# Performance work log

Measured on AMD Instinct MI355X. Metric: run time of the kernel, lower is better.

The kernel has to match this reference:

```python
import jax, jax.numpy as jnp
import numpy as np

VOCAB = 100000
EMBED = 64
HIDDEN = 256
SEQ = 200
BATCH = 4096


def setup_inputs() -> dict:
    key = jax.random.key(0)
    ks = jax.random.split(key, 12)
    s = 0.02
    return {
        "user_hist": jax.random.randint(ks[0], (BATCH, SEQ), 0, VOCAB),
        "target_item": jax.random.randint(ks[1], (BATCH,), 0, VOCAB),
        "user_emb": jax.random.normal(ks[2], (VOCAB, EMBED), jnp.float32) * s,
        "item_emb": jax.random.normal(ks[3], (VOCAB, EMBED), jnp.float32) * s,
        "attn_w1": jax.random.normal(ks[4], (4 * EMBED, HIDDEN), jnp.float32) * s,
        "attn_b1": jnp.zeros((HIDDEN,), jnp.float32),
        "attn_w2": jax.random.normal(ks[5], (HIDDEN, 1), jnp.float32) * s,
        "attn_b2": jnp.zeros((1,), jnp.float32),
        "mlp_w1": jax.random.normal(ks[6], (2 * EMBED, HIDDEN), jnp.float32) * s,
        "mlp_b1": jnp.zeros((HIDDEN,), jnp.float32),
        "mlp_w2": jax.random.normal(ks[7], (HIDDEN, 1), jnp.float32) * s,
        "mlp_b2": jnp.zeros((1,), jnp.float32),
    }


def reference(user_hist, target_item, user_emb, item_emb,
              attn_w1, attn_b1, attn_w2, attn_b2,
              mlp_w1, mlp_b1, mlp_w2, mlp_b2):
    # [B, S, E] history embeddings, [B, 1, E] target embedding
    h = user_emb[user_hist]
    t = item_emb[target_item][:, None, :]
    tb = jnp.broadcast_to(t, h.shape)
    # attention MLP over [B, S, 4E]
    att_in = jnp.concatenate([h, tb, h - t, h * t], axis=-1)
    att_h = jax.nn.relu(att_in @ attn_w1 + attn_b1)
    att_logits = (att_h @ attn_w2 + attn_b2)[..., 0]            # [B, S]
    att_w = jax.nn.softmax(att_logits, axis=-1)[..., None]      # [B, S, 1]
    user_interest = jnp.sum(h * att_w, axis=1)                  # [B, E]
    # prediction head on [B, 2E]
    mlp_in = jnp.concatenate([user_interest, t[:, 0, :]], axis=-1)
    mlp_h = jax.nn.relu(mlp_in @ mlp_w1 + mlp_b1)
    out = jax.nn.sigmoid(mlp_h @ mlp_w2 + mlp_b2)               # [B, 1]
    return out
```

## Files before the change

kernel.cpp:

```cpp
#include <hip/hip_runtime.h>
#include <math.h>

#define EMBED   64
#define HIDDEN  256
#define SEQ     200
#define SEQP    208
#define MT      13

typedef _Float16 f16x8  __attribute__((ext_vector_type(8)));
typedef float    f32x4  __attribute__((ext_vector_type(4)));
typedef float    f32x2  __attribute__((ext_vector_type(2)));

__global__ void din_precompute(const float* __restrict__ attn_w1,
                               const float* __restrict__ mlp_w1,
                               uint2* __restrict__ fragB8,
                               _Float16* __restrict__ fragW3,
                               _Float16* __restrict__ fragDt,
                               _Float16* __restrict__ fragB2) {
  const int gid = blockIdx.x * 256 + threadIdx.x;
  if (gid < 2048) {
    const int i = gid >> 7, rem = gid & 127, kc = rem >> 6, lane = rem & 63;
    const int n = i * 16 + (lane & 15);
    const int kb = kc * 32 + (lane >> 4) * 8;
    float v[8];
    #pragma unroll
    for (int j = 0; j < 8; ++j)
      v[j] = 16.0f * (attn_w1[(kb + j) * HIDDEN + n] + attn_w1[(128 + kb + j) * HIDDEN + n]);
    int lo = __builtin_amdgcn_cvt_pk_fp8_f32(v[0], v[1], 0, false);
    lo     = __builtin_amdgcn_cvt_pk_fp8_f32(v[2], v[3], lo, true);
    int hi = __builtin_amdgcn_cvt_pk_fp8_f32(v[4], v[5], 0, false);
    hi     = __builtin_amdgcn_cvt_pk_fp8_f32(v[6], v[7], hi, true);
    fragB8[gid] = uint2{(unsigned)lo, (unsigned)hi};
  } else if (gid < 4096) {
    const int g = gid - 2048;
    const int i = g >> 7, rem = g & 127, kc = rem >> 6, lane = rem & 63;
    const int n = i * 16 + (lane & 15);
    const int kb = kc * 32 + (lane >> 4) * 8;
    #pragma unroll
    for (int j = 0; j < 8; ++j)
      fragW3[g * 8 + j] = (_Float16)(16.0f * attn_w1[(192 + kb + j) * HIDDEN + n]);
  } else if (gid < 6144) {
    const int g = gid - 4096;
    const int i = g >> 7, rem = g & 127, kc = rem >> 6, lane = rem & 63;
    const int n = i * 16 + (lane & 15);
    const int kb = kc * 32 + (lane >> 4) * 8;
    #pragma unroll
    for (int j = 0; j < 8; ++j)
      fragDt[g * 8 + j] = (_Float16)(attn_w1[(64 + kb + j) * HIDDEN + n]
                                   - attn_w1[(128 + kb + j) * HIDDEN + n]);
  } else {
    const int g = gid - 6144;
    const int nt = g >> 8, kc = (g >> 6) & 3, lane = g & 63;
    const int n = nt * 16 + (lane & 15);
    const int kb = kc * 32 + (lane >> 4) * 8;
    #pragma unroll
    for (int j = 0; j < 8; ++j)
      fragB2[g * 8 + j] = (_Float16)mlp_w1[(kb + j) * HIDDEN + n];
  }
}

__global__ __launch_bounds__(512, 8)
void din_fused_kernel(const int* __restrict__ user_hist,
                      const int* __restrict__ target_item,
                      const float* __restrict__ user_emb,
                      const float* __restrict__ item_emb,
                      const float* __restrict__ attn_b1,
                      const float* __restrict__ attn_w2,
                      const float* __restrict__ mlp_b1,
                      const float* __restrict__ mlp_w2,
                      const float* __restrict__ mlp_b2,
                      const uint2* __restrict__ fragB8,
                      const _Float16* __restrict__ fragW3,
                      const _Float16* __restrict__ fragDt,
                      const _Float16* __restrict__ fragB2,
                      float* __restrict__ out)
{
  __shared__ __align__(16) uint2 Hf8[MT * 2 * 64];
  __shared__ __align__(16) _Float16 t16[EMBED];
  __shared__ int   histL[SEQP];
  __shared__ float lp[8][SEQP];
  __shared__ float weights[SEQP];
  __shared__ __align__(16) _Float16 mi16[EMBED];
  __shared__ float red[16];

  const int b    = blockIdx.x;
  const int tid  = threadIdx.x;
  const int lane = tid & 63;
  const int wave = tid >> 6;
  const int m    = lane & 15;
  const int quad = lane >> 4;

  if (tid < EMBED) t16[tid] = (_Float16)item_emb[target_item[b] * EMBED + tid];
  if (tid < SEQP) histL[tid] = (tid < SEQ) ? user_hist[b * SEQ + tid] : 0;

  long long Aw8[2][2];
  #pragma unroll
  for (int i = 0; i < 2; ++i)
    #pragma unroll
    for (int c = 0; c < 2; ++c)
      Aw8[i][c] = __builtin_bit_cast(long long, fragB8[((2 * wave + i) * 2 + c) * 64 + lane]);
  __syncthreads();

  for (int slot = tid; slot < MT * 2 * 64; slot += 512) {
    const int ln = slot & 63, kcomb = slot >> 6;
    const int st = kcomb >> 1, kc = kcomb & 1;
    const int s = st * 16 + (ln & 15);
    const int kb = kc * 32 + (ln >> 4) * 8;
    uint2 pv = uint2{0u, 0u};
    if (s < SEQ) {
      const float4* src = reinterpret_cast<const float4*>(&user_emb[histL[s] * EMBED + kb]);
      const float4 x = src[0], y = src[1];
      int lo = __builtin_amdgcn_cvt_pk_fp8_f32(16.f * x.x, 16.f * x.y, 0, false);
      lo     = __builtin_amdgcn_cvt_pk_fp8_f32(16.f * x.z, 16.f * x.w, lo, true);
      int hi = __builtin_amdgcn_cvt_pk_fp8_f32(16.f * y.x, 16.f * y.y, 0, false);
      hi     = __builtin_amdgcn_cvt_pk_fp8_f32(16.f * y.z, 16.f * y.w, hi, true);
      pv = uint2{(unsigned)lo, (unsigned)hi};
    }
    Hf8[slot] = pv;
  }
  __syncthreads();

  const f16x8 tv0 = *reinterpret_cast<const f16x8*>(&t16[quad * 8]);
  const f16x8 tv1 = *reinterpret_cast<const f16x8*>(&t16[32 + quad * 8]);

  long long AwT[2][2];
  #pragma unroll
  for (int i = 0; i < 2; ++i) {
    #pragma unroll
    for (int c = 0; c < 2; ++c) {
      const f16x8 w3v = reinterpret_cast<const f16x8*>(fragW3)[((2 * wave + i) * 2 + c) * 64 + lane];
      const f16x8 p = w3v * (c ? tv1 : tv0);
      int lo = __builtin_amdgcn_cvt_pk_fp8_f32((float)p[0], (float)p[1], 0, false);
      lo     = __builtin_amdgcn_cvt_pk_fp8_f32((float)p[2], (float)p[3], lo, true);
      int hi = __builtin_amdgcn_cvt_pk_fp8_f32((float)p[4], (float)p[5], 0, false);
      hi     = __builtin_amdgcn_cvt_pk_fp8_f32((float)p[6], (float)p[7], hi, true);
      AwT[i][c] = __builtin_bit_cast(long long, uint2{(unsigned)lo, (unsigned)hi});
    }
  }

  float cn[2][4], w2n[2][4];
  #pragma unroll
  for (int i = 0; i < 2; ++i) {
    const int tile = 2 * wave + i;
    const f16x8 d0 = reinterpret_cast<const f16x8*>(fragDt)[(tile * 2 + 0) * 64 + lane];
    const f16x8 d1 = reinterpret_cast<const f16x8*>(fragDt)[(tile * 2 + 1) * 64 + lane];
    f32x4 acc = {0.f, 0.f, 0.f, 0.f};
    acc = __builtin_amdgcn_mfma_f32_16x16x32_f16(d0, tv0, acc, 0, 0, 0);
    acc = __builtin_amdgcn_mfma_f32_16x16x32_f16(d1, tv1, acc, 0, 0, 0);
    const int nb = tile * 16 + quad * 4;
    const float4 b1v = *reinterpret_cast<const float4*>(&attn_b1[nb]);
    const float4 w2v = *reinterpret_cast<const float4*>(&attn_w2[nb]);
    cn[i][0] = 256.0f * (b1v.x + acc[0]);
    cn[i][1] = 256.0f * (b1v.y + acc[1]);
    cn[i][2] = 256.0f * (b1v.z + acc[2]);
    cn[i][3] = 256.0f * (b1v.w + acc[3]);
    w2n[i][0] = w2v.x * (1.0f / 256.0f);
    w2n[i][1] = w2v.y * (1.0f / 256.0f);
    w2n[i][2] = w2v.z * (1.0f / 256.0f);
    w2n[i][3] = w2v.w * (1.0f / 256.0f);
  }

  #pragma unroll 4
  for (int st = 0; st < MT; ++st) {
    const long long b0 = __builtin_bit_cast(long long, Hf8[(st * 2 + 0) * 64 + lane]);
    const long long b1 = __builtin_bit_cast(long long, Hf8[(st * 2 + 1) * 64 + lane]);
    float lg = 0.f;
    #pragma unroll
    for (int i = 0; i < 2; ++i) {
      f32x4 acc = {cn[i][0], cn[i][1], cn[i][2], cn[i][3]};
      acc = __builtin_amdgcn_mfma_f32_16x16x32_fp8_fp8(Aw8[i][0], b0, acc, 0, 0, 0);
      acc = __builtin_amdgcn_mfma_f32_16x16x32_fp8_fp8(Aw8[i][1], b1, acc, 0, 0, 0);
      acc = __builtin_amdgcn_mfma_f32_16x16x32_fp8_fp8(AwT[i][0], b0, acc, 0, 0, 0);
      acc = __builtin_amdgcn_mfma_f32_16x16x32_fp8_fp8(AwT[i][1], b1, acc, 0, 0, 0);
      #pragma unroll
      for (int r = 0; r < 4; ++r)
        lg += fmaxf(acc[r], 0.0f) * w2n[i][r];
    }
    lg += __shfl_xor(lg, 16, 64);
    lg += __shfl_xor(lg, 32, 64);
    if (lane < 16) lp[wave][st * 16 + lane] = lg;
  }
  __syncthreads();

  float v = -INFINITY, e = 0.0f;
  if (wave < 4) {
    if (tid < SEQ)
      v = lp[0][tid] + lp[1][tid] + lp[2][tid] + lp[3][tid]
        + lp[4][tid] + lp[5][tid] + lp[6][tid] + lp[7][tid];
    float mx = v;
    #pragma unroll
    for (int off = 32; off; off >>= 1) mx = fmaxf(mx, __shfl_xor(mx, off, 64));
    if (lane == 0) red[wave] = mx;
  }
  __syncthreads();
  if (wave < 4) {
    const float mx = fmaxf(fmaxf(red[0], red[1]), fmaxf(red[2], red[3]));
    e = (tid < SEQ) ? expf(v - mx) : 0.0f;
    float ssum = e;
    #pragma unroll
    for (int off = 32; off; off >>= 1) ssum += __shfl_xor(ssum, off, 64);
    if (lane == 0) red[4 + wave] = ssum;
  }
  __syncthreads();
  if (wave < 4) {
    const float tot = red[4] + red[5] + red[6] + red[7];
    if (tid < SEQP) weights[tid] = (tid < SEQ) ? e / tot : 0.0f;
  }
  __syncthreads();

  {
    const int kc = wave & 1, g = wave >> 1;
    float pk[8];
    #pragma unroll
    for (int j = 0; j < 8; ++j) pk[j] = 0.f;
    #pragma unroll
    for (int st2 = 0; st2 < 4; ++st2) {
      const int st = g + st2 * 4;
      if (st < MT) {
        const float wt = weights[st * 16 + m];
        const uint2 hv = Hf8[(st * 2 + kc) * 64 + lane];
        const f32x2 f0 = __builtin_amdgcn_cvt_pk_f32_fp8((int)hv.x, false);
        const f32x2 f1 = __builtin_amdgcn_cvt_pk_f32_fp8((int)hv.x, true);
        const f32x2 f2 = __builtin_amdgcn_cvt_pk_f32_fp8((int)hv.y, false);
        const f32x2 f3 = __builtin_amdgcn_cvt_pk_f32_fp8((int)hv.y, true);
        pk[0] += wt * f0.x;  pk[1] += wt * f0.y;
        pk[2] += wt * f1.x;  pk[3] += wt * f1.y;
        pk[4] += wt * f2.x;  pk[5] += wt * f2.y;
        pk[6] += wt * f3.x;  pk[7] += wt * f3.y;
      }
    }
    #pragma unroll
    for (int j = 0; j < 8; ++j) {
      float p = pk[j];
      p += __shfl_xor(p, 1, 64);
      p += __shfl_xor(p, 2, 64);
      p += __shfl_xor(p, 4, 64);
      p += __shfl_xor(p, 8, 64);
      pk[j] = p;
    }
    if (m == 0) {
      #pragma unroll
      for (int j = 0; j < 8; ++j)
        lp[g][kc * 32 + quad * 8 + j] = pk[j];
    }
  }
  __syncthreads();
  if (tid < EMBED)
    mi16[tid] = (_Float16)((lp[0][tid] + lp[1][tid] + lp[2][tid] + lp[3][tid]) * 0.0625f);
  __syncthreads();

  {
    const f16x8 mb0 = *reinterpret_cast<const f16x8*>(&mi16[quad * 8]);
    const f16x8 mb1 = *reinterpret_cast<const f16x8*>(&mi16[32 + quad * 8]);
    float z = 0.f;
    #pragma unroll
    for (int i = 0; i < 2; ++i) {
      const f16x8* B2 = reinterpret_cast<const f16x8*>(fragB2) + ((2 * wave + i) * 4) * 64 + lane;
      const int nb = (2 * wave + i) * 16 + quad * 4;
      const float4 bb = *reinterpret_cast<const float4*>(&mlp_b1[nb]);
      const float4 ww = *reinterpret_cast<const float4*>(&mlp_w2[nb]);
      f32x4 acc = {bb.x, bb.y, bb.z, bb.w};
      acc = __builtin_amdgcn_mfma_f32_16x16x32_f16(B2[0],   mb0, acc, 0, 0, 0);
      acc = __builtin_amdgcn_mfma_f32_16x16x32_f16(B2[64],  mb1, acc, 0, 0, 0);
      acc = __builtin_amdgcn_mfma_f32_16x16x32_f16(B2[128], tv0, acc, 0, 0, 0);
      acc = __builtin_amdgcn_mfma_f32_16x16x32_f16(B2[192], tv1, acc, 0, 0, 0);
      z += fmaxf(acc[0], 0.0f) * ww.x;
      z += fmaxf(acc[1], 0.0f) * ww.y;
      z += fmaxf(acc[2], 0.0f) * ww.z;
      z += fmaxf(acc[3], 0.0f) * ww.w;
    }
    z += __shfl_xor(z, 16, 64);
    z += __shfl_xor(z, 32, 64);
    if (lane == 0) red[wave] = z;
  }
  __syncthreads();
  if (tid == 0) {
    const float zz = red[0] + red[1] + red[2] + red[3]
                   + red[4] + red[5] + red[6] + red[7] + mlp_b2[0];
    out[b] = 1.0f / (1.0f + expf(-zz));
  }
}

extern "C" void kernel_launch(void* const* d_in, const int* in_sizes, int n_in,
                              void* d_out, int out_size, void* d_ws, size_t ws_size,
                              hipStream_t stream) {
  const int*   user_hist   = (const int*)  d_in[0];
  const int*   target_item = (const int*)  d_in[1];
  const float* user_emb    = (const float*)d_in[2];
  const float* item_emb    = (const float*)d_in[3];
  const float* attn_w1     = (const float*)d_in[4];
  const float* attn_b1     = (const float*)d_in[5];
  const float* attn_w2     = (const float*)d_in[6];
  const float* mlp_w1      = (const float*)d_in[8];
  const float* mlp_b1      = (const float*)d_in[9];
  const float* mlp_w2      = (const float*)d_in[10];
  const float* mlp_b2      = (const float*)d_in[11];
  float* out = (float*)d_out;

  uint2*    fragB8 = (uint2*)d_ws;
  _Float16* fragW3 = (_Float16*)((char*)d_ws + 16384);
  _Float16* fragDt = (_Float16*)((char*)d_ws + 49152);
  _Float16* fragB2 = (_Float16*)((char*)d_ws + 81920);

  din_precompute<<<40, 256, 0, stream>>>(attn_w1, mlp_w1, fragB8, fragW3, fragDt, fragB2);

  const int batch = in_sizes[1];
  din_fused_kernel<<<batch, 512, 0, stream>>>(
      user_hist, target_item, user_emb, item_emb,
      attn_b1, attn_w2, mlp_b1, mlp_w2, mlp_b2,
      fragB8, fragW3, fragDt, fragB2, out);
}
```

Before: 180.3 us.

## Use K=128 scaled FP8 MFMA with h*t operand folded into history tile

Replaces the four 16x16x32 fp8 MFMAs per tile with one 16x16x128 scaled f8f6f4 MFMA, moving the h*t product into the activation side so that each history row stores both h and h*t in fp8 in padded LDS rows. The prediction head also becomes a single K=128 fp8 MFMA with pre-packed weights, and the per-wave logit partials are reduced through LDS atomics instead of a lp buffer. Weight preprocessing is consolidated into fewer fragment arrays. This doubles the LDS history footprint and quantizes the head input to fp8, which risks accuracy and occupancy.

```diff
diff --git a/kernel.cpp b/kernel.cpp
--- a/kernel.cpp
+++ b/kernel.cpp
@@ -6,56 +6,56 @@
 #define SEQ     200
 #define SEQP    208
 #define MT      13
-
-typedef _Float16 f16x8  __attribute__((ext_vector_type(8)));
-typedef float    f32x4  __attribute__((ext_vector_type(4)));
-typedef float    f32x2  __attribute__((ext_vector_type(2)));
+#define HROW    80
+#define HHALF   (SEQP * HROW)
+
+typedef _Float16 f16x8 __attribute__((ext_vector_type(8)));
+typedef float    f32x4 __attribute__((ext_vector_type(4)));
+typedef float    f32x2 __attribute__((ext_vector_type(2)));
+typedef int      i32x8 __attribute__((ext_vector_type(8)));
 
 __global__ void din_precompute(const float* __restrict__ attn_w1,
                                const float* __restrict__ mlp_w1,
-                               uint2* __restrict__ fragB8,
-                               _Float16* __restrict__ fragW3,
-                               _Float16* __restrict__ fragDt,
-                               _Float16* __restrict__ fragB2) {
+                               uint4* __restrict__ fragA8,
+                               uint4* __restrict__ fragB28,
+                               _Float16* __restrict__ fragDt) {
   const int gid = blockIdx.x * 256 + threadIdx.x;
   if (gid < 2048) {
-    const int i = gid >> 7, rem = gid & 127, kc = rem >> 6, lane = rem & 63;
-    const int n = i * 16 + (lane & 15);
-    const int kb = kc * 32 + (lane >> 4) * 8;
-    float v[8];
-    #pragma unroll
-    for (int j = 0; j < 8; ++j)
-      v[j] = 16.0f * (attn_w1[(kb + j) * HIDDEN + n] + attn_w1[(128 + kb + j) * HIDDEN + n]);
-    int lo = __builtin_amdgcn_cvt_pk_fp8_f32(v[0], v[1], 0, false);
-    lo     = __builtin_amdgcn_cvt_pk_fp8_f32(v[2], v[3], lo, true);
-    int hi = __builtin_amdgcn_cvt_pk_fp8_f32(v[4], v[5], 0, false);
-    hi     = __builtin_amdgcn_cvt_pk_fp8_f32(v[6], v[7], hi, true);
-    fragB8[gid] = uint2{(unsigned)lo, (unsigned)hi};
-  } else if (gid < 4096) {
+    const bool head = gid >= 1024;
+    const int g = gid & 1023;
+    const int tile = g >> 6, lane = g & 63;
+    const int n = tile * 16 + (lane & 15);
+    const int q = lane >> 4;
+    float v[32];
+    #pragma unroll
+    for (int j = 0; j < 32; ++j) {
+      const int k = q * 32 + j;
+      if (head) {
+        v[j] = 16.0f * mlp_w1[k * HIDDEN + n];
+      } else {
+        if (k < 64) v[j] = 16.0f * (attn_w1[k * HIDDEN + n] + attn_w1[(128 + k) * HIDDEN + n]);
+        else        v[j] = 16.0f * attn_w1[(192 + (k - 64)) * HIDDEN + n];
+      }
+    }
+    unsigned d[8];
+    #pragma unroll
+    for (int w = 0; w < 8; ++w) {
+      int pk = __builtin_amdgcn_cvt_pk_fp8_f32(v[4 * w + 0], v[4 * w + 1], 0, false);
+      pk     = __builtin_amdgcn_cvt_pk_fp8_f32(v[4 * w + 2], v[4 * w + 3], pk, true);
+      d[w] = (unsigned)pk;
+    }
+    uint4* dst = (head ? fragB28 : fragA8) + (tile * 64 + lane) * 2;
+    dst[0] = uint4{d[0], d[1], d[2], d[3]};
+    dst[1] = uint4{d[4], d[5], d[6], d[7]};
+  } else {
     const int g = gid - 2048;
     const int i = g >> 7, rem = g & 127, kc = rem >> 6, lane = rem & 63;
     const int n = i * 16 + (lane & 15);
     const int kb = kc * 32 + (lane >> 4) * 8;
     #pragma unroll
     for (int j = 0; j < 8; ++j)
-      fragW3[g * 8 + j] = (_Float16)(16.0f * attn_w1[(192 + kb + j) * HIDDEN + n]);
-  } else if (gid < 6144) {
-    const int g = gid - 4096;
-    const int i = g >> 7, rem = g & 127, kc = rem >> 6, lane = rem & 63;
-    const int n = i * 16 + (lane & 15);
-    const int kb = kc * 32 + (lane >> 4) * 8;
-    #pragma unroll
-    for (int j = 0; j < 8; ++j)
       fragDt[g * 8 + j] = (_Float16)(attn_w1[(64 + kb + j) * HIDDEN + n]
                                    - attn_w1[(128 + kb + j) * HIDDEN + n]);
-  } else {
-    const int g = gid - 6144;
-    const int nt = g >> 8, kc = (g >> 6) & 3, lane = g & 63;
-    const int n = nt * 16 + (lane & 15);
-    const int kb = kc * 32 + (lane >> 4) * 8;
-    #pragma unroll
-    for (int j = 0; j < 8; ++j)
-      fragB2[g * 8 + j] = (_Float16)mlp_w1[(kb + j) * HIDDEN + n];
   }
 }
 
@@ -69,18 +69,19 @@
                       const float* __restrict__ mlp_b1,
                       const float* __restrict__ mlp_w2,
                       const float* __restrict__ mlp_b2,
-                      const uint2* __restrict__ fragB8,
-                      const _Float16* __restrict__ fragW3,
+                      const uint4* __restrict__ fragA8,
+                      const uint4* __restrict__ fragB28,
                       const _Float16* __restrict__ fragDt,
-                      const _Float16* __restrict__ fragB2,
                       float* __restrict__ out)
 {
-  __shared__ __align__(16) uint2 Hf8[MT * 2 * 64];
+  __shared__ __align__(16) unsigned char Hb8[2 * HHALF];
+  __shared__ float t32[EMBED];
   __shared__ __align__(16) _Float16 t16[EMBED];
+  __shared__ __align__(16) unsigned char xin8[128];
   __shared__ int   histL[SEQP];
-  __shared__ float lp[8][SEQP];
+  __shared__ float logits[SEQP];
   __shared__ float weights[SEQP];
-  __shared__ __align__(16) _Float16 mi16[EMBED];
+  __shared__ float pool[8][EMBED];
   __shared__ float red[16];
 
   const int b    = blockIdx.x;
@@ -90,15 +91,22 @@
   const int m    = lane & 15;
   const int quad = lane >> 4;
 
-  if (tid < EMBED) t16[tid] = (_Float16)item_emb[target_item[b] * EMBED + tid];
-  if (tid < SEQP) histL[tid] = (tid < SEQ) ? user_hist[b * SEQ + tid] : 0;
-
-  long long Aw8[2][2];
-  #pragma unroll
-  for (int i = 0; i < 2; ++i)
-    #pragma unroll
-    for (int c = 0; c < 2; ++c)
-      Aw8[i][c] = __builtin_bit_cast(long long, fragB8[((2 * wave + i) * 2 + c) * 64 + lane]);
+  const int tgt = target_item[b];
+  if (tid < EMBED) {
+    const float v = item_emb[tgt * EMBED + tid];
+    t32[tid] = v;
+    t16[tid] = (_Float16)v;
+  }
+  if (tid < 32) {
+    const float v0 = 16.0f * item_emb[tgt * EMBED + 2 * tid];
+    const float v1 = 16.0f * item_emb[tgt * EMBED + 2 * tid + 1];
+    const int pk = __builtin_amdgcn_cvt_pk_fp8_f32(v0, v1, 0, false);
+    *(short*)&xin8[64 + 2 * tid] = (short)(pk & 0xffff);
+  }
+  if (tid < SEQP) {
+    histL[tid]  = (tid < SEQ) ? user_hist[b * SEQ + tid] : 0;
+    logits[tid] = 0.0f;
+  }
   __syncthreads();
 
   for (int slot = tid; slot < MT * 2 * 64; slot += 512) {
@@ -106,38 +114,42 @@
     const int st = kcomb >> 1, kc = kcomb & 1;
     const int s = st * 16 + (ln & 15);
     const int kb = kc * 32 + (ln >> 4) * 8;
-    uint2 pv = uint2{0u, 0u};
+    const int off = s * HROW + kb;
     if (s < SEQ) {
       const float4* src = reinterpret_cast<const float4*>(&user_emb[histL[s] * EMBED + kb]);
-      const float4 x = src[0], y = src[1];
-      int lo = __builtin_amdgcn_cvt_pk_fp8_f32(16.f * x.x, 16.f * x.y, 0, false);
-      lo     = __builtin_amdgcn_cvt_pk_fp8_f32(16.f * x.z, 16.f * x.w, lo, true);
-      int hi = __builtin_amdgcn_cvt_pk_fp8_f32(16.f * y.x, 16.f * y.y, 0, false);
-      hi     = __builtin_amdgcn_cvt_pk_fp8_f32(16.f * y.z, 16.f * y.w, hi, true);
-      pv = uint2{(unsigned)lo, (unsigned)hi};
-    }
-    Hf8[slot] = pv;
+      float4 x = src[0], y = src[1];
+      x.x *= 16.f; x.y *= 16.f; x.z *= 16.f; x.w *= 16.f;
+      y.x *= 16.f; y.y *= 16.f; y.z *= 16.f; y.w *= 16.f;
+      int lo = __builtin_amdgcn_cvt_pk_fp8_f32(x.x, x.y, 0, false);
+      lo     = __builtin_amdgcn_cvt_pk_fp8_f32(x.z, x.w, lo, true);
+      int hi = __builtin_amdgcn_cvt_pk_fp8_f32(y.x, y.y, 0, false);
+      hi     = __builtin_amdgcn_cvt_pk_fp8_f32(y.z, y.w, hi, true);
+      const float4 ta = *reinterpret_cast<const float4*>(&t32[kb]);
+      const float4 tb = *reinterpret_cast<const float4*>(&t32[kb + 4]);
+      int lo2 = __builtin_amdgcn_cvt_pk_fp8_f32(x.x * ta.x, x.y * ta.y, 0, false);
+      lo2     = __builtin_amdgcn_cvt_pk_fp8_f32(x.z * ta.z, x.w * ta.w, lo2, true);
+      int hi2 = __builtin_amdgcn_cvt_pk_fp8_f32(y.x * tb.x, y.y * tb.y, 0, false);
+      hi2     = __builtin_amdgcn_cvt_pk_fp8_f32(y.z * tb.z, y.w * tb.w, hi2, true);
+      *(uint2*)&Hb8[off]         = uint2{(unsigned)lo,  (unsigned)hi};
+      *(uint2*)&Hb8[HHALF + off] = uint2{(unsigned)lo2, (unsigned)hi2};
+    } else {
+      *(uint2*)&Hb8[off]         = uint2{0u, 0u};
+      *(uint2*)&Hb8[HHALF + off] = uint2{0u, 0u};
+    }
+  }
+
+  i32x8 A8[2];
+  #pragma unroll
+  for (int i = 0; i < 2; ++i) {
+    const uint4 a0 = fragA8[((2 * wave + i) * 64 + lane) * 2 + 0];
+    const uint4 a1 = fragA8[((2 * wave + i) * 64 + lane) * 2 + 1];
+    A8[i] = i32x8{(int)a0.x, (int)a0.y, (int)a0.z, (int)a0.w,
+                  (int)a1.x, (int)a1.y, (int)a1.z, (int)a1.w};
   }
   __syncthreads();
 
   const f16x8 tv0 = *reinterpret_cast<const f16x8*>(&t16[quad * 8]);
   const f16x8 tv1 = *reinterpret_cast<const f16x8*>(&t16[32 + quad * 8]);
-
-  long long AwT[2][2];
-  #pragma unroll
-  for (int i = 0; i < 2; ++i) {
-    #pragma unroll
-    for (int c = 0; c < 2; ++c) {
-      const f16x8 w3v = reinterpret_cast<const f16x8*>(fragW3)[((2 * wave + i) * 2 + c) * 64 + lane];
-      const f16x8 p = w3v * (c ? tv1 : tv0);
-      int lo = __builtin_amdgcn_cvt_pk_fp8_f32((float)p[0], (float)p[1], 0, false);
-      lo     = __builtin_amdgcn_cvt_pk_fp8_f32((float)p[2], (float)p[3], lo, true);
-      int hi = __builtin_amdgcn_cvt_pk_fp8_f32((float)p[4], (float)p[5], 0, false);
-      hi     = __builtin_amdgcn_cvt_pk_fp8_f32((float)p[6], (float)p[7], hi, true);
-      AwT[i][c] = __builtin_bit_cast(long long, uint2{(unsigned)lo, (unsigned)hi});
-    }
-  }
-
   float cn[2][4], w2n[2][4];
   #pragma unroll
   for (int i = 0; i < 2; ++i) {
@@ -150,43 +162,39 @@
     const int nb = tile * 16 + quad * 4;
     const float4 b1v = *reinterpret_cast<const float4*>(&attn_b1[nb]);
     const float4 w2v = *reinterpret_cast<const float4*>(&attn_w2[nb]);
-    cn[i][0] = 256.0f * (b1v.x + acc[0]);
-    cn[i][1] = 256.0f * (b1v.y + acc[1]);
-    cn[i][2] = 256.0f * (b1v.z + acc[2]);
-    cn[i][3] = 256.0f * (b1v.w + acc[3]);
-    w2n[i][0] = w2v.x * (1.0f / 256.0f);
-    w2n[i][1] = w2v.y * (1.0f / 256.0f);
-    w2n[i][2] = w2v.z * (1.0f / 256.0f);
-    w2n[i][3] = w2v.w * (1.0f / 256.0f);
-  }
-
-  #pragma unroll 4
-  for (int st = 0; st < MT; ++st) {
-    const long long b0 = __builtin_bit_cast(long long, Hf8[(st * 2 + 0) * 64 + lane]);
-    const long long b1 = __builtin_bit_cast(long long, Hf8[(st * 2 + 1) * 64 + lane]);
-    float lg = 0.f;
-    #pragma unroll
-    for (int i = 0; i < 2; ++i) {
-      f32x4 acc = {cn[i][0], cn[i][1], cn[i][2], cn[i][3]};
-      acc = __builtin_amdgcn_mfma_f32_16x16x32_fp8_fp8(Aw8[i][0], b0, acc, 0, 0, 0);
-      acc = __builtin_amdgcn_mfma_f32_16x16x32_fp8_fp8(Aw8[i][1], b1, acc, 0, 0, 0);
-      acc = __builtin_amdgcn_mfma_f32_16x16x32_fp8_fp8(AwT[i][0], b0, acc, 0, 0, 0);
-      acc = __builtin_amdgcn_mfma_f32_16x16x32_fp8_fp8(AwT[i][1], b1, acc, 0, 0, 0);
+    cn[i][0] = b1v.x + acc[0];  cn[i][1] = b1v.y + acc[1];
+    cn[i][2] = b1v.z + acc[2];  cn[i][3] = b1v.w + acc[3];
+    w2n[i][0] = w2v.x; w2n[i][1] = w2v.y; w2n[i][2] = w2v.z; w2n[i][3] = w2v.w;
+  }
+
+  {
+    const unsigned char* hb = Hb8 + (quad >> 1) * HHALF + (quad & 1) * 32 + m * HROW;
+    for (int st = 0; st < MT; ++st) {
+      const uint4 b0 = *reinterpret_cast<const uint4*>(hb + st * 16 * HROW);
+      const uint4 b1 = *reinterpret_cast<const uint4*>(hb + st * 16 * HROW + 16);
+      const i32x8 B8 = i32x8{(int)b0.x, (int)b0.y, (int)b0.z, (int)b0.w,
+                             (int)b1.x, (int)b1.y, (int)b1.z, (int)b1.w};
+      float lg = 0.f;
       #pragma unroll
-      for (int r = 0; r < 4; ++r)
-        lg += fmaxf(acc[r], 0.0f) * w2n[i][r];
-    }
-    lg += __shfl_xor(lg, 16, 64);
-    lg += __shfl_xor(lg, 32, 64);
-    if (lane < 16) lp[wave][st * 16 + lane] = lg;
+      for (int i = 0; i < 2; ++i) {
+        f32x4 acc = {cn[i][0], cn[i][1], cn[i][2], cn[i][3]};
+        acc = __builtin_amdgcn_mfma_scale_f32_16x16x128_f8f6f4(
+                  A8[i], B8, acc, 0, 0, 0, 0x77777777, 0, 0x7F7F7F7F);
+        lg += fmaxf(acc[0], 0.0f) * w2n[i][0];
+        lg += fmaxf(acc[1], 0.0f) * w2n[i][1];
+        lg += fmaxf(acc[2], 0.0f) * w2n[i][2];
+        lg += fmaxf(acc[3], 0.0f) * w2n[i][3];
+      }
+      lg += __shfl_xor(lg, 16, 64);
+      lg += __shfl_xor(lg, 32, 64);
+      if (lane < 16) atomicAdd(&logits[st * 16 + lane], lg);
+    }
   }
   __syncthreads();
 
   float v = -INFINITY, e = 0.0f;
   if (wave < 4) {
-    if (tid < SEQ)
-      v = lp[0][tid] + lp[1][tid] + lp[2][tid] + lp[3][tid]
-        + lp[4][tid] + lp[5][tid] + lp[6][tid] + lp[7][tid];
+    if (tid < SEQ) v = logits[tid];
     float mx = v;
     #pragma unroll
     for (int off = 32; off; off >>= 1) mx = fmaxf(mx, __shfl_xor(mx, off, 64));
@@ -209,61 +217,61 @@
   __syncthreads();
 
   {
-    const int kc = wave & 1, g = wave >> 1;
-    float pk[8];
-    #pragma unroll
-    for (int j = 0; j < 8; ++j) pk[j] = 0.f;
-    #pragma unroll
-    for (int st2 = 0; st2 < 4; ++st2) {
-      const int st = g + st2 * 4;
-      if (st < MT) {
-        const float wt = weights[st * 16 + m];
-        const uint2 hv = Hf8[(st * 2 + kc) * 64 + lane];
-        const f32x2 f0 = __builtin_amdgcn_cvt_pk_f32_fp8((int)hv.x, false);
-        const f32x2 f1 = __builtin_amdgcn_cvt_pk_f32_fp8((int)hv.x, true);
-        const f32x2 f2 = __builtin_amdgcn_cvt_pk_f32_fp8((int)hv.y, false);
-        const f32x2 f3 = __builtin_amdgcn_cvt_pk_f32_fp8((int)hv.y, true);
-        pk[0] += wt * f0.x;  pk[1] += wt * f0.y;
-        pk[2] += wt * f1.x;  pk[3] += wt * f1.y;
-        pk[4] += wt * f2.x;  pk[5] += wt * f2.y;
-        pk[6] += wt * f3.x;  pk[7] += wt * f3.y;
-      }
-    }
-    #pragma unroll
-    for (int j = 0; j < 8; ++j) {
-      float p = pk[j];
-      p += __shfl_xor(p, 1, 64);
-      p += __shfl_xor(p, 2, 64);
-      p += __shfl_xor(p, 4, 64);
-      p += __shfl_xor(p, 8, 64);
-      pk[j] = p;
-    }
-    if (m == 0) {
-      #pragma unroll
-      for (int j = 0; j < 8; ++j)
-        lp[g][kc * 32 + quad * 8 + j] = pk[j];
-    }
-  }
-  __syncthreads();
-  if (tid < EMBED)
-    mi16[tid] = (_Float16)((lp[0][tid] + lp[1][tid] + lp[2][tid] + lp[3][tid]) * 0.0625f);
+    const int kd = m;
+    const int s0 = wave * 4 + quad;
+    float pk4[4] = {0.f, 0.f, 0.f, 0.f};
+    for (int s = s0; s < SEQ; s += 32) {
+      const float wt = weights[s];
+      const unsigned hv = *reinterpret_cast<const unsigned*>(&Hb8[s * HROW + kd * 4]);
+      const f32x2 f0 = __builtin_amdgcn_cvt_pk_f32_fp8((int)hv, false);
+      const f32x2 f1 = __builtin_amdgcn_cvt_pk_f32_fp8((int)hv, true);
+      pk4[0] += wt * f0.x;  pk4[1] += wt * f0.y;
+      pk4[2] += wt * f1.x;  pk4[3] += wt * f1.y;
+    }
+    #pragma unroll
+    for (int j = 0; j < 4; ++j) {
+      float p = pk4[j];
+      p += __shfl_xor(p, 16, 64);
+      p += __shfl_xor(p, 32, 64);
+      pk4[j] = p;
+    }
+    if (quad == 0)
+      *reinterpret_cast<float4*>(&pool[wave][kd * 4]) = float4{pk4[0], pk4[1], pk4[2], pk4[3]};
+  }
+  __syncthreads();
+  if (tid < 32) {
+    const int k0 = 2 * tid;
+    float a = 0.f, c = 0.f;
+    #pragma unroll
+    for (int w = 0; w < 8; ++w) { a += pool[w][k0]; c += pool[w][k0 + 1]; }
+    const int pk = __builtin_amdgcn_cvt_pk_fp8_f32(a, c, 0, false);
+    *(short*)&xin8[k0] = (short)(pk & 0xffff);
+  }
   __syncthreads();
 
   {
-    const f16x8 mb0 = *reinterpret_cast<const f16x8*>(&mi16[quad * 8]);
-    const f16x8 mb1 = *reinterpret_cast<const f16x8*>(&mi16[32 + quad * 8]);
+    i32x8 A2[2];
+    #pragma unroll
+    for (int i = 0; i < 2; ++i) {
+      const uint4 a0 = fragB28[((2 * wave + i) * 64 + lane) * 2 + 0];
+      const uint4 a1 = fragB28[((2 * wave + i) * 64 + lane) * 2 + 1];
+      A2[i] = i32x8{(int)a0.x, (int)a0.y, (int)a0.z, (int)a0.w,
+                    (int)a1.x, (int)a1.y, (int)a1.z, (int)a1.w};
+    }
+    const int xo = (quad >> 1) * 64 + (quad & 1) * 32;
+    const uint4 b0 = *reinterpret_cast<const uint4*>(&xin8[xo]);
+    const uint4 b1 = *reinterpret_cast<const uint4*>(&xin8[xo + 16]);
+    const i32x8 B2 = i32x8{(int)b0.x, (int)b0.y, (int)b0.z, (int)b0.w,
+                           (int)b1.x, (int)b1.y, (int)b1.z, (int)b1.w};
     float z = 0.f;
     #pragma unroll
     for (int i = 0; i < 2; ++i) {
-      const f16x8* B2 = reinterpret_cast<const f16x8*>(fragB2) + ((2 * wave + i) * 4) * 64 + lane;
       const int nb = (2 * wave + i) * 16 + quad * 4;
       const float4 bb = *reinterpret_cast<const float4*>(&mlp_b1[nb]);
       const float4 ww = *reinterpret_cast<const float4*>(&mlp_w2[nb]);
       f32x4 acc = {bb.x, bb.y, bb.z, bb.w};
-      acc = __builtin_amdgcn_mfma_f32_16x16x32_f16(B2[0],   mb0, acc, 0, 0, 0);
-      acc = __builtin_amdgcn_mfma_f32_16x16x32_f16(B2[64],  mb1, acc, 0, 0, 0);
-      acc = __builtin_amdgcn_mfma_f32_16x16x32_f16(B2[128], tv0, acc, 0, 0, 0);
-      acc = __builtin_amdgcn_mfma_f32_16x16x32_f16(B2[192], tv1, acc, 0, 0, 0);
+      acc = __builtin_amdgcn_mfma_scale_f32_16x16x128_f8f6f4(
+                A2[i], B2, acc, 0, 0, 0, 0x77777777, 0, 0x7F7F7F7F);
       z += fmaxf(acc[0], 0.0f) * ww.x;
       z += fmaxf(acc[1], 0.0f) * ww.y;
       z += fmaxf(acc[2], 0.0f) * ww.z;
@@ -297,16 +305,15 @@
   const float* mlp_b2      = (const float*)d_in[11];
   float* out = (float*)d_out;
 
-  uint2*    fragB8 = (uint2*)d_ws;
-  _Float16* fragW3 = (_Float16*)((char*)d_ws + 16384);
-  _Float16* fragDt = (_Float16*)((char*)d_ws + 49152);
-  _Float16* fragB2 = (_Float16*)((char*)d_ws + 81920);
-
-  din_precompute<<<40, 256, 0, stream>>>(attn_w1, mlp_w1, fragB8, fragW3, fragDt, fragB2);
+  uint4*    fragA8  = (uint4*)d_ws;
+  uint4*    fragB28 = (uint4*)((char*)d_ws + 32768);
+  _Float16* fragDt  = (_Float16*)((char*)d_ws + 65536);
+
+  din_precompute<<<16, 256, 0, stream>>>(attn_w1, mlp_w1, fragA8, fragB28, fragDt);
 
   const int batch = in_sizes[1];
   din_fused_kernel<<<batch, 512, 0, stream>>>(
       user_hist, target_item, user_emb, item_emb,
       attn_b1, attn_w2, mlp_b1, mlp_w2, mlp_b2,
-      fragB8, fragW3, fragDt, fragB2, out);
+      fragA8, fragB28, fragDt, out);
 }
```

After: 199.2 us. 10.5% more time.

## Pre-convert user embedding table to FP8 once and gather bytes instead of floats

Applied to the files above, without the earlier changes.

Adds a kernel that converts the whole user_emb table (100000x64) to scaled FP8 in the workspace before the fused kernel runs. The fused kernel then gathers 8-byte FP8 chunks per slot instead of two float4 loads plus conversion, which cuts the gather traffic by about four times. The cost is a full-table pass per call (about 25.6 MB read and 6.4 MB written), which may exceed what the gather saves. The sync is moved to after the weight setup and the main-loop unroll goes from 4 to 2. It falls back to the old path if the workspace is too small.

```diff
diff --git a/kernel.cpp b/kernel.cpp
--- a/kernel.cpp
+++ b/kernel.cpp
@@ -6,6 +6,7 @@
 #define SEQ     200
 #define SEQP    208
 #define MT      13
+#define VOCAB   100000
 
 typedef _Float16 f16x8  __attribute__((ext_vector_type(8)));
 typedef float    f32x4  __attribute__((ext_vector_type(4)));
@@ -57,6 +58,18 @@
     for (int j = 0; j < 8; ++j)
       fragB2[g * 8 + j] = (_Float16)mlp_w1[(kb + j) * HIDDEN + n];
   }
+}
+
+__global__ void din_emb8(const float* __restrict__ user_emb, unsigned char* __restrict__ emb8) {
+  const int g = blockIdx.x * 256 + threadIdx.x;
+  const int base = g * 8;
+  const float4 x = *reinterpret_cast<const float4*>(&user_emb[base]);
+  const float4 y = *reinterpret_cast<const float4*>(&user_emb[base + 4]);
+  int lo = __builtin_amdgcn_cvt_pk_fp8_f32(16.f * x.x, 16.f * x.y, 0, false);
+  lo     = __builtin_amdgcn_cvt_pk_fp8_f32(16.f * x.z, 16.f * x.w, lo, true);
+  int hi = __builtin_amdgcn_cvt_pk_fp8_f32(16.f * y.x, 16.f * y.y, 0, false);
+  hi     = __builtin_amdgcn_cvt_pk_fp8_f32(16.f * y.z, 16.f * y.w, hi, true);
+  *reinterpret_cast<uint2*>(&emb8[base]) = uint2{(unsigned)lo, (unsigned)hi};
 }
 
 __global__ __launch_bounds__(512, 8)
@@ -73,6 +86,7 @@
                       const _Float16* __restrict__ fragW3,
                       const _Float16* __restrict__ fragDt,
                       const _Float16* __restrict__ fragB2,
+                      const unsigned char* __restrict__ emb8,
                       float* __restrict__ out)
 {
   __shared__ __align__(16) uint2 Hf8[MT * 2 * 64];
@@ -101,24 +115,36 @@
       Aw8[i][c] = __builtin_bit_cast(long long, fragB8[((2 * wave + i) * 2 + c) * 64 + lane]);
   __syncthreads();
 
-  for (int slot = tid; slot < MT * 2 * 64; slot += 512) {
-    const int ln = slot & 63, kcomb = slot >> 6;
-    const int st = kcomb >> 1, kc = kcomb & 1;
-    const int s = st * 16 + (ln & 15);
-    const int kb = kc * 32 + (ln >> 4) * 8;
-    uint2 pv = uint2{0u, 0u};
-    if (s < SEQ) {
-      const float4* src = reinterpret_cast<const float4*>(&user_emb[histL[s] * EMBED + kb]);
-      const float4 x = src[0], y = src[1];
-      int lo = __builtin_amdgcn_cvt_pk_fp8_f32(16.f * x.x, 16.f * x.y, 0, false);
-      lo     = __builtin_amdgcn_cvt_pk_fp8_f32(16.f * x.z, 16.f * x.w, lo, true);
-      int hi = __builtin_amdgcn_cvt_pk_fp8_f32(16.f * y.x, 16.f * y.y, 0, false);
-      hi     = __builtin_amdgcn_cvt_pk_fp8_f32(16.f * y.z, 16.f * y.w, hi, true);
-      pv = uint2{(unsigned)lo, (unsigned)hi};
-    }
-    Hf8[slot] = pv;
-  }
-  __syncthreads();
+  if (emb8) {
+    for (int slot = tid; slot < MT * 2 * 64; slot += 512) {
+      const int ln = slot & 63, kcomb = slot >> 6;
+      const int st = kcomb >> 1, kc = kcomb & 1;
+      const int s = st * 16 + (ln & 15);
+      const int kb = kc * 32 + (ln >> 4) * 8;
+      uint2 pv = uint2{0u, 0u};
+      if (s < SEQ)
+        pv = *reinterpret_cast<const uint2*>(&emb8[histL[s] * EMBED + kb]);
+      Hf8[slot] = pv;
+    }
+  } else {
+    for (int slot = tid; slot < MT * 2 * 64; slot += 512) {
+      const int ln = slot & 63, kcomb = slot >> 6;
+      const int st = kcomb >> 1, kc = kcomb & 1;
+      const int s = st * 16 + (ln & 15);
+      const int kb = kc * 32 + (ln >> 4) * 8;
+      uint2 pv = uint2{0u, 0u};
+      if (s < SEQ) {
+        const float4* src = reinterpret_cast<const float4*>(&user_emb[histL[s] * EMBED + kb]);
+        const float4 x = src[0], y = src[1];
+        int lo = __builtin_amdgcn_cvt_pk_fp8_f32(16.f * x.x, 16.f * x.y, 0, false);
+        lo     = __builtin_amdgcn_cvt_pk_fp8_f32(16.f * x.z, 16.f * x.w, lo, true);
+        int hi = __builtin_amdgcn_cvt_pk_fp8_f32(16.f * y.x, 16.f * y.y, 0, false);
+        hi     = __builtin_amdgcn_cvt_pk_fp8_f32(16.f * y.z, 16.f * y.w, hi, true);
+        pv = uint2{(unsigned)lo, (unsigned)hi};
+      }
+      Hf8[slot] = pv;
+    }
+  }
 
   const f16x8 tv0 = *reinterpret_cast<const f16x8*>(&t16[quad * 8]);
   const f16x8 tv1 = *reinterpret_cast<const f16x8*>(&t16[32 + quad * 8]);
@@ -159,8 +185,9 @@
     w2n[i][2] = w2v.z * (1.0f / 256.0f);
     w2n[i][3] = w2v.w * (1.0f / 256.0f);
   }
-
-  #pragma unroll 4
+  __syncthreads();
+
+  #pragma unroll 2
   for (int st = 0; st < MT; ++st) {
     const long long b0 = __builtin_bit_cast(long long, Hf8[(st * 2 + 0) * 64 + lane]);
     const long long b1 = __builtin_bit_cast(long long, Hf8[(st * 2 + 1) * 64 + lane]);
@@ -301,12 +328,19 @@
   _Float16* fragW3 = (_Float16*)((char*)d_ws + 16384);
   _Float16* fragDt = (_Float16*)((char*)d_ws + 49152);
   _Float16* fragB2 = (_Float16*)((char*)d_ws + 81920);
+  const size_t emb8_off = 147456;
+  const size_t emb8_bytes = (size_t)VOCAB * EMBED;
+  unsigned char* emb8 = nullptr;
+  if (ws_size >= emb8_off + emb8_bytes)
+    emb8 = (unsigned char*)d_ws + emb8_off;
 
   din_precompute<<<40, 256, 0, stream>>>(attn_w1, mlp_w1, fragB8, fragW3, fragDt, fragB2);
+  if (emb8)
+    din_emb8<<<(VOCAB * EMBED / 8 + 255) / 256, 256, 0, stream>>>(user_emb, emb8);
 
   const int batch = in_sizes[1];
   din_fused_kernel<<<batch, 512, 0, stream>>>(
       user_hist, target_item, user_emb, item_emb,
       attn_b1, attn_w2, mlp_b1, mlp_w2, mlp_b2,
-      fragB8, fragW3, fragDt, fragB2, out);
+      fragB8, fragW3, fragDt, fragB2, emb8, out);
 }
```

After: 176.0 us. 2.4% less time.
